# Kernel tuning notes

Hardware: AMD Instinct MI355X
Metric: run time of the kernel (lower is better)

Reference implementation:

```python
import jax, jax.numpy as jnp
import numpy as np
import math

F_DIM = 64
N_NODES = 2048
N_HEADS = 4
HEAD_DIM = F_DIM // N_HEADS
C_DIM = 8
FUSION_WEIGHT = 1e-05
LN_EPS = 1e-5
BATCH = 4


def setup_inputs() -> dict:
    key = jax.random.key(0)
    ks = jax.random.split(key, 16)

    def xavier(k, shape):
        fan_in, fan_out = shape[-2], shape[-1]
        lim = math.sqrt(6.0 / (fan_in + fan_out))
        return jax.random.uniform(k, shape, jnp.float32, -lim, lim)

    return {
        "features": jax.random.normal(ks[0], (BATCH, N_NODES, F_DIM), jnp.float32),
        "fixed_graph": jax.random.uniform(ks[1], (N_NODES, N_NODES), jnp.float32),
        "learned_graph": jax.random.uniform(ks[2], (BATCH, N_NODES, N_NODES), jnp.float32),
        # qkv_compress: Linear(F, 3C); qkv_expand: Linear(3C, 3F)
        "Wqc": xavier(ks[3], (F_DIM, 3 * C_DIM)),
        "bqc": jnp.zeros((3 * C_DIM,), jnp.float32),
        "Wqe": xavier(ks[4], (3 * C_DIM, 3 * F_DIM)),
        "bqe": jnp.zeros((3 * F_DIM,), jnp.float32),
        # output_compress: Linear(F, C); output_expand: Linear(C, F)
        "Woc": xavier(ks[5], (F_DIM, C_DIM)),
        "boc": jnp.zeros((C_DIM,), jnp.float32),
        "Woe": xavier(ks[6], (C_DIM, F_DIM)),
        "boe": jnp.zeros((F_DIM,), jnp.float32),
        # learned structure bias factors [H,N,C] @ [H,C,N]
        "bf1": xavier(ks[7], (N_HEADS, N_NODES, C_DIM)),
        "bf2": xavier(ks[8], (N_HEADS, C_DIM, N_NODES)),
        "graph_fusion": jnp.array([0.5], jnp.float32),
        "ln_g": jnp.ones((F_DIM,), jnp.float32),
        "ln_b": jnp.zeros((F_DIM,), jnp.float32),
    }


def _layernorm(x, g, b):
    mu = jnp.mean(x, axis=-1, keepdims=True)
    var = jnp.mean(jnp.square(x - mu), axis=-1, keepdims=True)
    return (x - mu) * jax.lax.rsqrt(var + LN_EPS) * g + b


def reference(features, fixed_graph, learned_graph, Wqc, bqc, Wqe, bqe,
              Woc, boc, Woe, boe, bf1, bf2, graph_fusion, ln_g, ln_b):
    B, N, F = features.shape
    H, hd = N_HEADS, HEAD_DIM
    residual = features

    # compressed QKV projection: [B,N,F] -> [B,N,3C] -> [B,N,3F]
    qkv = (features @ Wqc + bqc) @ Wqe + bqe
    q, k, v = jnp.split(qkv, 3, axis=-1)
    # [B,N,F] -> [B,H,N,hd]
    to_heads = lambda x: x.reshape(B, N, H, hd).transpose(0, 2, 1, 3)
    q, k, v = to_heads(q), to_heads(k), to_heads(v)

    # attention scores + learned low-rank structure bias [H,N,N]
    scores = jnp.einsum("bhnd,bhmd->bhnm", q, k) / math.sqrt(hd)
    scores = scores + jnp.einsum("hnc,hcm->hnm", bf1, bf2)

    # graph fusion: sigmoid-weighted blend of learned and fixed graphs
    fr = jax.nn.sigmoid(graph_fusion[0])
    combined = fr * learned_graph + (1.0 - fr) * fixed_graph[None, :, :]  # [B,N,N]
    scores = scores + combined[:, None, :, :]

    attn = jax.nn.softmax(scores, axis=-1)  # dropout is identity in eval mode
    context = jnp.einsum("bhnm,bhmd->bhnd", attn, v)
    context = context.transpose(0, 2, 1, 3).reshape(B, N, F)

    out = (context @ Woc + boc) @ Woe + boe
    out = _layernorm(out + residual, ln_g, ln_b)

    reg_loss = FUSION_WEIGHT * jnp.mean(jnp.abs(attn))
    return out, reg_loss
```

## Files before the change

### kernel.cpp

```cpp
#include <hip/hip_runtime.h>
#include <hip/hip_bf16.h>

#define BB 4
#define NN 2048
#define NH 4
#define HDD 16
#define FD 64
#define SPLIT 8
#define KPB (NN / SPLIT)
#define KT (KPB / 64)
#define PADK 17
#define L2E 1.44269504088896f

typedef __attribute__((ext_vector_type(8))) short bf16x8;
typedef __attribute__((ext_vector_type(4))) float f32x4;

union BW { __hip_bfloat16 b; unsigned short u; };

static __device__ inline unsigned pk2(float a, float b) {
    BW x, y;
    x.b = __float2bfloat16(a);
    y.b = __float2bfloat16(b);
    return (unsigned)x.u | ((unsigned)y.u << 16);
}

static __device__ inline float wsum(float v) {
    v += __shfl_xor(v, 1);  v += __shfl_xor(v, 2);  v += __shfl_xor(v, 4);
    v += __shfl_xor(v, 8);  v += __shfl_xor(v, 16); v += __shfl_xor(v, 32);
    return v;
}

__global__ __launch_bounds__(256) void fuse_kernel(
    const float* __restrict__ Wqc, const float* __restrict__ bqc,
    const float* __restrict__ Wqe, const float* __restrict__ bqe,
    const float* __restrict__ Woc, const float* __restrict__ boc,
    const float* __restrict__ Woe, const float* __restrict__ boe,
    float* __restrict__ W1, float* __restrict__ b1,
    float* __restrict__ W2, float* __restrict__ b2)
{
    const int t = threadIdx.x;
    if (blockIdx.x == 0) {
        for (int idx = t; idx < 64 * 192; idx += 256) {
            const int r = idx / 192, c = idx - r * 192;
            float a = 0.f;
            #pragma unroll
            for (int j = 0; j < 24; ++j) a += Wqc[r * 24 + j] * Wqe[j * 192 + c];
            if (c < 64) a *= 0.25f * L2E;
            W1[idx] = a;
        }
        if (t < 192) {
            float a = bqe[t];
            #pragma unroll
            for (int j = 0; j < 24; ++j) a += bqc[j] * Wqe[j * 192 + t];
            if (t < 64) a *= 0.25f * L2E;
            b1[t] = a;
        }
    } else {
        for (int idx = t; idx < 64 * 64; idx += 256) {
            const int r = idx >> 6, c = idx & 63;
            float a = 0.f;
            #pragma unroll
            for (int j = 0; j < 8; ++j) a += Woc[r * 8 + j] * Woe[j * 64 + c];
            W2[idx] = a;
        }
        if (t < 64) {
            float a = boe[t];
            #pragma unroll
            for (int j = 0; j < 8; ++j) a += boc[j] * Woe[j * 64 + t];
            b2[t] = a;
        }
    }
}

__global__ __launch_bounds__(256) void qkv_kernel(
    const float* __restrict__ feat,
    const float* __restrict__ W1, const float* __restrict__ b1,
    const float* __restrict__ bf1, const float* __restrict__ bf2,
    __hip_bfloat16* __restrict__ Qe, __hip_bfloat16* __restrict__ Ke,
    __hip_bfloat16* __restrict__ Vt)
{
    __shared__ float fl[4][64];
    const int t = threadIdx.x;
    const int w = t >> 6, lane = t & 63;
    const int bn = blockIdx.x * 4 + w;
    const int b = bn >> 11, n = bn & (NN - 1);

    fl[w][lane] = feat[(size_t)bn * FD + lane];
    __syncthreads();

    float v0 = b1[lane], v1 = b1[lane + 64], v2 = b1[lane + 128];
    #pragma unroll 8
    for (int d = 0; d < 64; ++d) {
        const float f = fl[w][d];
        v0 += f * W1[d * 192 + lane];
        v1 += f * W1[d * 192 + 64 + lane];
        v2 += f * W1[d * 192 + 128 + lane];
    }

    const int h = lane >> 4, hi = lane & 15;
    const size_t rowQ = (((size_t)b * NH + h) * NN + n) * 32;
    Qe[rowQ + hi] = __float2bfloat16(v0);
    Ke[rowQ + hi] = __float2bfloat16(v1);
    Vt[(((size_t)b * NH + h) * HDD + hi) * NN + n] = __float2bfloat16(v2);

    if (lane < 32) {
        const int hh = lane >> 3, c = lane & 7;
        const size_t r = (((size_t)b * NH + hh) * NN + n) * 32;
        Qe[r + 16 + c] = __float2bfloat16(bf1[((size_t)hh * NN + n) * 8 + c] * L2E);
        Qe[r + 24 + c] = __float2bfloat16(0.f);
    } else {
        const int hh = (lane - 32) >> 3, c = lane & 7;
        const size_t r = (((size_t)b * NH + hh) * NN + n) * 32;
        Ke[r + 16 + c] = __float2bfloat16(bf2[((size_t)hh * 8 + c) * NN + n]);
        Ke[r + 24 + c] = __float2bfloat16(0.f);
    }
}

__global__ __launch_bounds__(256, 8) void attn_kernel(
    const float* __restrict__ fixedg, const float* __restrict__ learng,
    const float* __restrict__ gfus,
    const __hip_bfloat16* __restrict__ Qe, const __hip_bfloat16* __restrict__ Ke,
    const __hip_bfloat16* __restrict__ Vt,
    float* __restrict__ pacc, float* __restrict__ psum)
{
    __shared__ float lds[2 * 64 * PADK];

    const int bid = blockIdx.x;
    const int split = bid & (SPLIT - 1);
    const int qt = (bid >> 3) & 127;
    const int b = bid >> 10;
    const int qb = qt << 4;
    const int kbase = split * KPB;
    const int t = threadIdx.x;
    const int hw = t >> 6;
    const int lane = t & 63;
    const int ql = lane & 15;
    const int g  = lane >> 4;

    const float sg = 1.f / (1.f + __expf(-gfus[0]));
    const float fre = sg * L2E, ofre = (1.f - sg) * L2E;

    const size_t bhN = ((size_t)b * NH + hw) * NN;
    const bf16x8 qf = *(const bf16x8*)(Qe + (bhN + qb + ql) * 32 + g * 8);
    const __hip_bfloat16* kptr = Ke + bhN * 32;
    const __hip_bfloat16* vbase = Vt + (((size_t)b * NH + hw) * HDD + ql) * NN;
    const int krow = 8 * (ql >> 2) + (ql & 3);

    const int sq = t >> 4;
    const int sk = (t & 15) * 4;
    const float* lrow = learng + ((size_t)b * NN + qb + sq) * NN + kbase + sk;
    const float* frow = fixedg + ((size_t)(qb + sq)) * NN + kbase + sk;

    float ssum = 0.f;
    f32x4 acc = {0.f, 0.f, 0.f, 0.f};

    f32x4 lw[2], fw[2];
    lw[0] = *(const f32x4*)(lrow);
    fw[0] = *(const f32x4*)(frow);

    #pragma unroll
    for (int kt = 0; kt < KT; ++kt) {
        const int cur = kt & 1, nxt = cur ^ 1;
        if (kt + 1 < KT) {
            lw[nxt] = *(const f32x4*)(lrow + (kt + 1) * 64);
            fw[nxt] = *(const f32x4*)(frow + (kt + 1) * 64);
        }
        float* dst = lds + cur * (64 * PADK);
        #pragma unroll
        for (int i = 0; i < 4; ++i)
            dst[(sk + i) * PADK + sq] = fre * lw[cur][i] + ofre * fw[cur][i];
        __syncthreads();

        const float* cmb = lds + cur * (64 * PADK);
        #pragma unroll
        for (int hf = 0; hf < 2; ++hf) {
            const int kb = kbase + kt * 64 + hf * 32;
            const bf16x8 k0 = *(const bf16x8*)(kptr + (size_t)(kb + krow) * 32 + g * 8);
            const bf16x8 k1 = *(const bf16x8*)(kptr + (size_t)(kb + 4 + krow) * 32 + g * 8);
            const f32x4 z = {0.f, 0.f, 0.f, 0.f};
            f32x4 c0 = __builtin_amdgcn_mfma_f32_16x16x32_bf16(k0, qf, z, 0, 0, 0);
            f32x4 c1 = __builtin_amdgcn_mfma_f32_16x16x32_bf16(k1, qf, z, 0, 0, 0);
            const int lk = hf * 32 + 8 * g;
            #pragma unroll
            for (int j = 0; j < 4; ++j) {
                c0[j] = __builtin_amdgcn_exp2f(c0[j] + cmb[(lk + j) * PADK + ql]);
                c1[j] = __builtin_amdgcn_exp2f(c1[j] + cmb[(lk + 4 + j) * PADK + ql]);
                ssum += c0[j] + c1[j];
            }
            union { unsigned u[4]; bf16x8 v; } pf;
            pf.u[0] = pk2(c0[0], c0[1]);
            pf.u[1] = pk2(c0[2], c0[3]);
            pf.u[2] = pk2(c1[0], c1[1]);
            pf.u[3] = pk2(c1[2], c1[3]);
            const bf16x8 vf = *(const bf16x8*)(vbase + kb + 8 * g);
            acc = __builtin_amdgcn_mfma_f32_16x16x32_bf16(vf, pf.v, acc, 0, 0, 0);
        }
    }

    ssum += __shfl_xor(ssum, 16);
    ssum += __shfl_xor(ssum, 32);
    if (g == 0)
        psum[((size_t)(split * BB + b) * NH + hw) * NN + qb + ql] = ssum;

    float* ldsO = lds;
    #pragma unroll
    for (int j = 0; j < 4; ++j) ldsO[ql * 68 + hw * 16 + 4 * g + j] = acc[j];
    __syncthreads();
    for (int q2 = hw; q2 < 16; q2 += 4)
        pacc[((size_t)(split * BB + b) * NN + qb + q2) * FD + lane] = ldsO[q2 * 68 + lane];
}

__global__ __launch_bounds__(256) void out_kernel(
    const float* __restrict__ pacc, const float* __restrict__ psum,
    const float* __restrict__ feat,
    const float* __restrict__ W2, const float* __restrict__ b2,
    const float* __restrict__ lng, const float* __restrict__ lnb,
    float* __restrict__ out)
{
    __shared__ float cl[4][64];
    const int t = threadIdx.x;
    const int w = t >> 6, d = t & 63;
    const int node = blockIdx.x * 4 + w;
    const int b = node >> 11, n = node & (NN - 1);
    const int h = d >> 4;

    float a = 0.f, sh = 0.f;
    #pragma unroll
    for (int sp = 0; sp < SPLIT; ++sp) {
        a  += pacc[((size_t)sp * BB * NN + node) * FD + d];
        sh += psum[((size_t)(sp * BB + b) * NH + h) * NN + n];
    }
    cl[w][d] = a / sh;
    __syncthreads();

    float o = b2[d];
    #pragma unroll 8
    for (int dd = 0; dd < 64; ++dd) o += cl[w][dd] * W2[dd * 64 + d];
    o += feat[(size_t)node * FD + d];

    const float mu = wsum(o) * (1.f / 64.f);
    const float df = o - mu;
    const float va = wsum(df * df) * (1.f / 64.f);
    out[(size_t)node * FD + d] = df * rsqrtf(va + 1e-5f) * lng[d] + lnb[d];
    if (blockIdx.x == 0 && t == 0)
        out[(size_t)BB * NN * FD] = 4.8828125e-9f;
}

extern "C" void kernel_launch(void* const* d_in, const int* in_sizes, int n_in,
                              void* d_out, int out_size, void* d_ws, size_t ws_size,
                              hipStream_t stream) {
    const float* feat   = (const float*)d_in[0];
    const float* fixedg = (const float*)d_in[1];
    const float* learng = (const float*)d_in[2];
    const float* Wqc = (const float*)d_in[3];
    const float* bqc = (const float*)d_in[4];
    const float* Wqe = (const float*)d_in[5];
    const float* bqe = (const float*)d_in[6];
    const float* Woc = (const float*)d_in[7];
    const float* boc = (const float*)d_in[8];
    const float* Woe = (const float*)d_in[9];
    const float* boe = (const float*)d_in[10];
    const float* bf1 = (const float*)d_in[11];
    const float* bf2 = (const float*)d_in[12];
    const float* gfus = (const float*)d_in[13];
    const float* lng = (const float*)d_in[14];
    const float* lnb = (const float*)d_in[15];

    char* ws = (char*)d_ws;
    __hip_bfloat16* Qe = (__hip_bfloat16*)ws;
    __hip_bfloat16* Ke = Qe + (size_t)BB * NH * NN * 32;
    __hip_bfloat16* Vt = Ke + (size_t)BB * NH * NN * 32;
    float* pacc = (float*)(Vt + (size_t)BB * NH * HDD * NN);
    float* psum = pacc + (size_t)SPLIT * BB * NN * FD;
    float* W1 = psum + (size_t)SPLIT * BB * NH * NN;
    float* b1 = W1 + 64 * 192;
    float* W2 = b1 + 192;
    float* b2 = W2 + 64 * 64;
    float* out = (float*)d_out;

    hipLaunchKernelGGL(fuse_kernel, dim3(2), dim3(256), 0, stream,
                       Wqc, bqc, Wqe, bqe, Woc, boc, Woe, boe, W1, b1, W2, b2);
    hipLaunchKernelGGL(qkv_kernel, dim3(BB * NN / 4), dim3(256), 0, stream,
                       feat, W1, b1, bf1, bf2, Qe, Ke, Vt);
    hipLaunchKernelGGL(attn_kernel, dim3(BB * (NN / 16) * SPLIT), dim3(256), 0, stream,
                       fixedg, learng, gfus, Qe, Ke, Vt, pacc, psum);
    hipLaunchKernelGGL(out_kernel, dim3(BB * NN / 4), dim3(256), 0, stream,
                       pacc, psum, feat, W2, b2, lng, lnb, out);
}
```

Before: 216.9 us.

## Double query tile per block to reuse K/V loads and vectorize graph staging

Each attention block now handles 32 query rows instead of 16, so every K and V fragment it loads is used for two query sub-tiles (two sets of MFMAs and accumulators). The combined-graph tile in LDS is now stored row-major with 8-wide vector loads and stores instead of a transposed scalar layout. The store for the next tile is moved after the compute, with a single barrier per iteration. The kernel also writes 8-wide vectorized output rows to pacc. The block count is halved and launch bounds drop to 4 waves per SIMD, which trades occupancy for register reuse. The kernel is still bound by reading the two dense NxN graphs.

```diff
diff --git a/kernel.cpp b/kernel.cpp
--- a/kernel.cpp
+++ b/kernel.cpp
@@ -6,10 +6,11 @@
 #define NH 4
 #define HDD 16
 #define FD 64
+#define QB 32
 #define SPLIT 8
 #define KPB (NN / SPLIT)
 #define KT (KPB / 64)
-#define PADK 17
+#define CS 68
 #define L2E 1.44269504088896f
 
 typedef __attribute__((ext_vector_type(8))) short bf16x8;
@@ -116,20 +117,20 @@
     }
 }
 
-__global__ __launch_bounds__(256, 8) void attn_kernel(
+__global__ __launch_bounds__(256, 4) void attn_kernel(
     const float* __restrict__ fixedg, const float* __restrict__ learng,
     const float* __restrict__ gfus,
     const __hip_bfloat16* __restrict__ Qe, const __hip_bfloat16* __restrict__ Ke,
     const __hip_bfloat16* __restrict__ Vt,
     float* __restrict__ pacc, float* __restrict__ psum)
 {
-    __shared__ float lds[2 * 64 * PADK];
+    __shared__ float lds[2 * QB * CS];
 
     const int bid = blockIdx.x;
     const int split = bid & (SPLIT - 1);
-    const int qt = (bid >> 3) & 127;
-    const int b = bid >> 10;
-    const int qb = qt << 4;
+    const int qt = (bid >> 3) & 63;
+    const int b = bid >> 9;
+    const int qb = qt << 5;
     const int kbase = split * KPB;
     const int t = threadIdx.x;
     const int hw = t >> 6;
@@ -141,73 +142,98 @@
     const float fre = sg * L2E, ofre = (1.f - sg) * L2E;
 
     const size_t bhN = ((size_t)b * NH + hw) * NN;
-    const bf16x8 qf = *(const bf16x8*)(Qe + (bhN + qb + ql) * 32 + g * 8);
+    const bf16x8 qfA = *(const bf16x8*)(Qe + (bhN + qb + ql) * 32 + g * 8);
+    const bf16x8 qfB = *(const bf16x8*)(Qe + (bhN + qb + 16 + ql) * 32 + g * 8);
     const __hip_bfloat16* kptr = Ke + bhN * 32;
     const __hip_bfloat16* vbase = Vt + (((size_t)b * NH + hw) * HDD + ql) * NN;
     const int krow = 8 * (ql >> 2) + (ql & 3);
 
-    const int sq = t >> 4;
-    const int sk = (t & 15) * 4;
+    const int sq = t >> 3;
+    const int sk = (t & 7) * 8;
     const float* lrow = learng + ((size_t)b * NN + qb + sq) * NN + kbase + sk;
     const float* frow = fixedg + ((size_t)(qb + sq)) * NN + kbase + sk;
 
-    float ssum = 0.f;
-    f32x4 acc = {0.f, 0.f, 0.f, 0.f};
-
-    f32x4 lw[2], fw[2];
-    lw[0] = *(const f32x4*)(lrow);
-    fw[0] = *(const f32x4*)(frow);
+    float ssA = 0.f, ssB = 0.f;
+    f32x4 accA = {0.f, 0.f, 0.f, 0.f}, accB = {0.f, 0.f, 0.f, 0.f};
+    f32x4 l0, l1, f0, f1;
+
+    l0 = *(const f32x4*)(lrow);      l1 = *(const f32x4*)(lrow + 4);
+    f0 = *(const f32x4*)(frow);      f1 = *(const f32x4*)(frow + 4);
+    *(f32x4*)&lds[sq * CS + sk]     = fre * l0 + ofre * f0;
+    *(f32x4*)&lds[sq * CS + sk + 4] = fre * l1 + ofre * f1;
 
     #pragma unroll
     for (int kt = 0; kt < KT; ++kt) {
-        const int cur = kt & 1, nxt = cur ^ 1;
+        __syncthreads();
         if (kt + 1 < KT) {
-            lw[nxt] = *(const f32x4*)(lrow + (kt + 1) * 64);
-            fw[nxt] = *(const f32x4*)(frow + (kt + 1) * 64);
-        }
-        float* dst = lds + cur * (64 * PADK);
-        #pragma unroll
-        for (int i = 0; i < 4; ++i)
-            dst[(sk + i) * PADK + sq] = fre * lw[cur][i] + ofre * fw[cur][i];
-        __syncthreads();
-
-        const float* cmb = lds + cur * (64 * PADK);
+            l0 = *(const f32x4*)(lrow + (kt + 1) * 64);
+            l1 = *(const f32x4*)(lrow + (kt + 1) * 64 + 4);
+            f0 = *(const f32x4*)(frow + (kt + 1) * 64);
+            f1 = *(const f32x4*)(frow + (kt + 1) * 64 + 4);
+        }
+        const float* cmb = lds + (kt & 1) * (QB * CS);
         #pragma unroll
         for (int hf = 0; hf < 2; ++hf) {
             const int kb = kbase + kt * 64 + hf * 32;
             const bf16x8 k0 = *(const bf16x8*)(kptr + (size_t)(kb + krow) * 32 + g * 8);
             const bf16x8 k1 = *(const bf16x8*)(kptr + (size_t)(kb + 4 + krow) * 32 + g * 8);
             const f32x4 z = {0.f, 0.f, 0.f, 0.f};
-            f32x4 c0 = __builtin_amdgcn_mfma_f32_16x16x32_bf16(k0, qf, z, 0, 0, 0);
-            f32x4 c1 = __builtin_amdgcn_mfma_f32_16x16x32_bf16(k1, qf, z, 0, 0, 0);
-            const int lk = hf * 32 + 8 * g;
+            f32x4 cA0 = __builtin_amdgcn_mfma_f32_16x16x32_bf16(k0, qfA, z, 0, 0, 0);
+            f32x4 cA1 = __builtin_amdgcn_mfma_f32_16x16x32_bf16(k1, qfA, z, 0, 0, 0);
+            f32x4 cB0 = __builtin_amdgcn_mfma_f32_16x16x32_bf16(k0, qfB, z, 0, 0, 0);
+            f32x4 cB1 = __builtin_amdgcn_mfma_f32_16x16x32_bf16(k1, qfB, z, 0, 0, 0);
+            const int col = hf * 32 + 8 * g;
+            const f32x4 gA0 = *(const f32x4*)&cmb[ql * CS + col];
+            const f32x4 gA1 = *(const f32x4*)&cmb[ql * CS + col + 4];
+            const f32x4 gB0 = *(const f32x4*)&cmb[(ql + 16) * CS + col];
+            const f32x4 gB1 = *(const f32x4*)&cmb[(ql + 16) * CS + col + 4];
             #pragma unroll
             for (int j = 0; j < 4; ++j) {
-                c0[j] = __builtin_amdgcn_exp2f(c0[j] + cmb[(lk + j) * PADK + ql]);
-                c1[j] = __builtin_amdgcn_exp2f(c1[j] + cmb[(lk + 4 + j) * PADK + ql]);
-                ssum += c0[j] + c1[j];
+                cA0[j] = __builtin_amdgcn_exp2f(cA0[j] + gA0[j]);
+                cA1[j] = __builtin_amdgcn_exp2f(cA1[j] + gA1[j]);
+                cB0[j] = __builtin_amdgcn_exp2f(cB0[j] + gB0[j]);
+                cB1[j] = __builtin_amdgcn_exp2f(cB1[j] + gB1[j]);
+                ssA += cA0[j] + cA1[j];
+                ssB += cB0[j] + cB1[j];
             }
-            union { unsigned u[4]; bf16x8 v; } pf;
-            pf.u[0] = pk2(c0[0], c0[1]);
-            pf.u[1] = pk2(c0[2], c0[3]);
-            pf.u[2] = pk2(c1[0], c1[1]);
-            pf.u[3] = pk2(c1[2], c1[3]);
+            union { unsigned u[4]; bf16x8 v; } pfA, pfB;
+            pfA.u[0] = pk2(cA0[0], cA0[1]);  pfA.u[1] = pk2(cA0[2], cA0[3]);
+            pfA.u[2] = pk2(cA1[0], cA1[1]);  pfA.u[3] = pk2(cA1[2], cA1[3]);
+            pfB.u[0] = pk2(cB0[0], cB0[1]);  pfB.u[1] = pk2(cB0[2], cB0[3]);
+            pfB.u[2] = pk2(cB1[0], cB1[1]);  pfB.u[3] = pk2(cB1[2], cB1[3]);
             const bf16x8 vf = *(const bf16x8*)(vbase + kb + 8 * g);
-            acc = __builtin_amdgcn_mfma_f32_16x16x32_bf16(vf, pf.v, acc, 0, 0, 0);
-        }
-    }
-
-    ssum += __shfl_xor(ssum, 16);
-    ssum += __shfl_xor(ssum, 32);
-    if (g == 0)
-        psum[((size_t)(split * BB + b) * NH + hw) * NN + qb + ql] = ssum;
+            accA = __builtin_amdgcn_mfma_f32_16x16x32_bf16(vf, pfA.v, accA, 0, 0, 0);
+            accB = __builtin_amdgcn_mfma_f32_16x16x32_bf16(vf, pfB.v, accB, 0, 0, 0);
+        }
+        if (kt + 1 < KT) {
+            float* dst = lds + ((kt + 1) & 1) * (QB * CS);
+            *(f32x4*)&dst[sq * CS + sk]     = fre * l0 + ofre * f0;
+            *(f32x4*)&dst[sq * CS + sk + 4] = fre * l1 + ofre * f1;
+        }
+    }
+
+    ssA += __shfl_xor(ssA, 16);  ssA += __shfl_xor(ssA, 32);
+    ssB += __shfl_xor(ssB, 16);  ssB += __shfl_xor(ssB, 32);
+    if (g == 0) {
+        psum[((size_t)(split * BB + b) * NH + hw) * NN + qb + ql] = ssA;
+        psum[((size_t)(split * BB + b) * NH + hw) * NN + qb + 16 + ql] = ssB;
+    }
 
     float* ldsO = lds;
     #pragma unroll
-    for (int j = 0; j < 4; ++j) ldsO[ql * 68 + hw * 16 + 4 * g + j] = acc[j];
+    for (int j = 0; j < 4; ++j) {
+        ldsO[ql * CS + hw * 16 + 4 * g + j] = accA[j];
+        ldsO[(ql + 16) * CS + hw * 16 + 4 * g + j] = accB[j];
+    }
     __syncthreads();
-    for (int q2 = hw; q2 < 16; q2 += 4)
-        pacc[((size_t)(split * BB + b) * NN + qb + q2) * FD + lane] = ldsO[q2 * 68 + lane];
+    {
+        const int r = t >> 3, c = (t & 7) * 8;
+        const f32x4 o0 = *(const f32x4*)&ldsO[r * CS + c];
+        const f32x4 o1 = *(const f32x4*)&ldsO[r * CS + c + 4];
+        float* prow = pacc + ((size_t)(split * BB + b) * NN + qb + r) * FD + c;
+        *(f32x4*)prow = o0;
+        *(f32x4*)(prow + 4) = o1;
+    }
 }
 
 __global__ __launch_bounds__(256) void out_kernel(
@@ -282,7 +308,7 @@
                        Wqc, bqc, Wqe, bqe, Woc, boc, Woe, boe, W1, b1, W2, b2);
     hipLaunchKernelGGL(qkv_kernel, dim3(BB * NN / 4), dim3(256), 0, stream,
                        feat, W1, b1, bf1, bf2, Qe, Ke, Vt);
-    hipLaunchKernelGGL(attn_kernel, dim3(BB * (NN / 16) * SPLIT), dim3(256), 0, stream,
+    hipLaunchKernelGGL(attn_kernel, dim3(BB * (NN / QB) * SPLIT), dim3(256), 0, stream,
                        fixedg, learng, gfus, Qe, Ke, Vt, pacc, psum);
     hipLaunchKernelGGL(out_kernel, dim3(BB * NN / 4), dim3(256), 0, stream,
                        pacc, psum, feat, W2, b2, lng, lnb, out);
```

Result: faster. 206.4 us (-4.8%).
